# Kernel optimization log

Measured on AMD Instinct MI355X. Metric: run time of the kernel, lower is better.

Reference implementation:

```python
import jax, jax.numpy as jnp
import numpy as np
import math

N, B, D, K = 2000, 2000, 32, 3  # nodes, bills, dim, order+1


def setup_inputs() -> dict:
    key = jax.random.key(0)
    ks = jax.random.split(key, 6)
    return {
        "events": jax.random.randint(ks[0], (N, B), 0, 2) > 0,          # [N,B] bool votes
        "events_time": jax.random.uniform(ks[1], (B,), dtype=jnp.float32),  # [B] bill times
        "beta": jax.random.uniform(ks[2], (B,), dtype=jnp.float32),     # bill bias
        "gamma": jax.random.uniform(ks[3], (N,), dtype=jnp.float32),    # politician bias
        "z_b": jax.random.uniform(ks[4], (B, D), dtype=jnp.float32),    # bill embeddings
        "z_p": jax.random.uniform(ks[5], (K, N, D), dtype=jnp.float32), # stacked order-o politician coeffs
    }


def reference(events, events_time, beta, gamma, z_b, z_p):
    k = z_p.shape[0]
    inv_fact = jnp.asarray([1.0 / math.factorial(o) for o in range(k)], dtype=z_p.dtype)
    # powers[o, b] = t_b**o  (o=0 handled explicitly so grads are safe at t=0)
    powers = jnp.stack(
        [jnp.ones_like(events_time) if o == 0 else events_time ** o for o in range(k)]
    )  # [K,B]
    coeff = powers * inv_fact[:, None]                     # [K,B]  t^o/o!
    pos = jnp.einsum('kb,knd->bnd', coeff, z_p)            # [B,N,D] politician positions at each bill time
    diff = pos - z_b[:, None, :]                           # [B,N,D]
    dist = jnp.sqrt(jnp.sum(diff * diff, axis=-1))         # [B,N] Euclidean distance
    logits = gamma[None, :] + beta[:, None] - dist         # [B,N]
    # log p if voted, log(1-p) otherwise; log(1-sigmoid(x)) == log_sigmoid(-x)
    ll = jnp.where(events.T, jax.nn.log_sigmoid(logits), jax.nn.log_sigmoid(-logits))
    return -jnp.sum(ll)
```

## Files before the change

kernel.cpp:

```cpp
#include <hip/hip_runtime.h>
#include <hip/hip_fp16.h>
#include <math.h>

#define NN    2000
#define NB    2000
#define DD    32
#define NOCT  16
#define TILE  64
#define GDIM  32
#define NPART (GDIM * GDIM)

typedef _Float16 half8   __attribute__((ext_vector_type(8)));
typedef float    float4v __attribute__((ext_vector_type(4)));

__global__ __launch_bounds__(256, 4) void pol2vec_main(
    const int*   __restrict__ events,
    const float* __restrict__ tarr,
    const float* __restrict__ beta,
    const float* __restrict__ gamma,
    const float* __restrict__ zb,
    const float* __restrict__ zp,
    float*       __restrict__ partials)
{
    __shared__ _Float16 sW[NOCT * TILE * 8];
    __shared__ _Float16 sZ[NOCT * TILE * 8];
    __shared__ float    sT[TILE][4][6];
    __shared__ float    sT2[TILE][4];
    __shared__ float    s_red[4];

    const int tid  = threadIdx.x;
    const int lane = tid & 63;
    const int w    = tid >> 6;
    const int b0   = blockIdx.x * TILE;
    const int n0   = blockIdx.y * TILE;
    const int wr   = (w >> 1) * 32;
    const int wc   = (w & 1) * 32;
    const int l15  = lane & 15;
    const int l4   = lane >> 4;

    unsigned evb = 0u, vb = 0u;
#pragma unroll
    for (int nr = 0; nr < 2; ++nr)
#pragma unroll
    for (int bc = 0; bc < 2; ++bc)
#pragma unroll
    for (int r = 0; r < 4; ++r) {
        const int ng = n0 + wr + 16 * nr + l4 * 4 + r;
        const int bg = b0 + wc + 16 * bc + l15;
        const bool v = (ng < NN) && (bg < NB);
        const size_t idx = v ? ((size_t)ng * NB + bg) : 0;
        const unsigned bit = 1u << (nr * 8 + bc * 4 + r);
        if (v) vb |= bit;
        if (v && events[idx]) evb |= bit;
    }

    for (int u = tid; u < NOCT * TILE; u += 256) {
        const int oct = u >> 6, nl = u & 63;
        const int n = n0 + nl;
        half8 hv = {};
        if (oct < 12 && n < NN) {
            const float* src = zp + ((size_t)(oct >> 2) * NN + n) * DD + 8 * (oct & 3);
            const float4 x = ((const float4*)src)[0];
            const float4 y = ((const float4*)src)[1];
            hv[0] = (_Float16)x.x; hv[1] = (_Float16)x.y;
            hv[2] = (_Float16)x.z; hv[3] = (_Float16)x.w;
            hv[4] = (_Float16)y.x; hv[5] = (_Float16)y.y;
            hv[6] = (_Float16)y.z; hv[7] = (_Float16)y.w;
        }
        *(half8*)(sW + (size_t)u * 8) = hv;
    }
    for (int u = tid; u < NOCT * TILE; u += 256) {
        const int oct = u >> 6, bl = u & 63;
        const int b = b0 + bl;
        half8 hv = {};
        if (oct < 12 && b < NB) {
            const float t = tarr[b];
            const float s = (oct < 4) ? 1.f : (oct < 8) ? t : 0.5f * t * t;
            const float* src = zb + (size_t)b * DD + 8 * (oct & 3);
            const float4 x = ((const float4*)src)[0];
            const float4 y = ((const float4*)src)[1];
            hv[0] = (_Float16)(s * x.x); hv[1] = (_Float16)(s * x.y);
            hv[2] = (_Float16)(s * x.z); hv[3] = (_Float16)(s * x.w);
            hv[4] = (_Float16)(s * y.x); hv[5] = (_Float16)(s * y.y);
            hv[6] = (_Float16)(s * y.z); hv[7] = (_Float16)(s * y.w);
        }
        *(half8*)(sZ + (size_t)u * 8) = hv;
    }

    {
        const int nl = tid >> 2, q = tid & 3;
        const int n = n0 + nl;
        float aa = 0.f, ab = 0.f, ac = 0.f, bb = 0.f, bc2 = 0.f, cc6 = 0.f;
        if (n < NN) {
            const float* pA = zp + (size_t)n * DD + 8 * q;
            const float* pB = zp + ((size_t)NN + n) * DD + 8 * q;
            const float* pC = zp + ((size_t)2 * NN + n) * DD + 8 * q;
#pragma unroll
            for (int d = 0; d < 8; ++d) {
                const float a = pA[d], b = pB[d], c = pC[d];
                aa = fmaf(a, a, aa); ab = fmaf(a, b, ab); ac = fmaf(a, c, ac);
                bb = fmaf(b, b, bb); bc2 = fmaf(b, c, bc2); cc6 = fmaf(c, c, cc6);
            }
        }
        sT[nl][q][0] = aa;  sT[nl][q][1] = ab;  sT[nl][q][2] = ac;
        sT[nl][q][3] = bb;  sT[nl][q][4] = bc2; sT[nl][q][5] = cc6;
    }
    {
        const int bl = tid >> 2, q = tid & 3;
        const int b = b0 + bl;
        float z2p = 0.f;
        if (b < NB) {
            const float* zr = zb + (size_t)b * DD + 8 * q;
#pragma unroll
            for (int d = 0; d < 8; ++d) z2p = fmaf(zr[d], zr[d], z2p);
        }
        sT2[bl][q] = z2p;
    }
    __syncthreads();

    if (tid < TILE) {
        const int nl = tid;
        float c6[6];
#pragma unroll
        for (int i = 0; i < 6; ++i)
            c6[i] = (sT[nl][0][i] + sT[nl][1][i]) + (sT[nl][2][i] + sT[nl][3][i]);
        half8 hv = {};
        hv[0] = (_Float16)c6[0];
        hv[1] = (_Float16)(2.f * c6[1]);
        hv[2] = (_Float16)(c6[3] + c6[2]);
        hv[3] = (_Float16)c6[4];
        hv[4] = (_Float16)(0.25f * c6[5]);
        hv[5] = (_Float16)1.f;
        *(half8*)(sW + ((size_t)12 * TILE + nl) * 8) = hv;
    } else if (tid < 2 * TILE) {
        const int bl = tid - TILE;
        const int b = b0 + bl;
        const float z2 = (sT2[bl][0] + sT2[bl][1]) + (sT2[bl][2] + sT2[bl][3]);
        const float t = (b < NB) ? tarr[b] : 0.f;
        const float t2 = t * t;
        half8 hv = {};
        hv[0] = (_Float16)(-0.5f);
        hv[1] = (_Float16)(-0.5f * t);
        hv[2] = (_Float16)(-0.5f * t2);
        hv[3] = (_Float16)(-0.5f * t2 * t);
        hv[4] = (_Float16)(-0.5f * t2 * t2);
        hv[5] = (_Float16)(-0.5f * z2);
        *(half8*)(sZ + ((size_t)12 * TILE + bl) * 8) = hv;
    }
    __syncthreads();

    half8 af[2][4], bf[2][4];
#pragma unroll
    for (int ks = 0; ks < 4; ++ks) {
        const int oct = 4 * ks + l4;
#pragma unroll
        for (int h = 0; h < 2; ++h) {
            af[h][ks] = *(const half8*)(sW + ((size_t)oct * TILE + wr + 16 * h + l15) * 8);
            bf[h][ks] = *(const half8*)(sZ + ((size_t)oct * TILE + wc + 16 * h + l15) * 8);
        }
    }

    float4v acc[2][2] = {};
#pragma unroll
    for (int nr = 0; nr < 2; ++nr)
#pragma unroll
    for (int bc = 0; bc < 2; ++bc)
#pragma unroll
    for (int ks = 0; ks < 4; ++ks)
        acc[nr][bc] = __builtin_amdgcn_mfma_f32_16x16x32_f16(
            af[nr][ks], bf[bc][ks], acc[nr][bc], 0, 0, 0);

    float accs = 0.f;
#pragma unroll
    for (int bc = 0; bc < 2; ++bc) {
        const int bg = b0 + wc + 16 * bc + l15;
        const float be = beta[bg < NB ? bg : 0];
#pragma unroll
        for (int nr = 0; nr < 2; ++nr) {
#pragma unroll
            for (int r = 0; r < 4; ++r) {
                const int ng = n0 + wr + 16 * nr + l4 * 4 + r;
                const float g = gamma[ng < NN ? ng : 0];
                const float d2 = fmaxf(-2.f * acc[nr][bc][r], 0.f);
                const float L  = g + be - sqrtf(d2);
                const unsigned bit = 1u << (nr * 8 + bc * 4 + r);
                const float sgn = (evb & bit) ? 1.f : -1.f;
                const float s   = sgn * L;
                const float term = fmaxf(-s, 0.f) + __logf(1.f + __expf(-fabsf(s)));
                accs += (vb & bit) ? term : 0.f;
            }
        }
    }

#pragma unroll
    for (int o = 32; o > 0; o >>= 1) accs += __shfl_down(accs, o, 64);
    if (lane == 0) s_red[w] = accs;
    __syncthreads();
    if (tid == 0)
        partials[blockIdx.y * GDIM + blockIdx.x] =
            (s_red[0] + s_red[1]) + (s_red[2] + s_red[3]);
}

__global__ __launch_bounds__(256) void pol2vec_reduce(
    const float4* __restrict__ p4, float* __restrict__ out)
{
    __shared__ float s_red[4];
    const int tid = threadIdx.x;
    const float4 v = p4[tid];
    float s = (v.x + v.y) + (v.z + v.w);
#pragma unroll
    for (int o = 32; o > 0; o >>= 1) s += __shfl_down(s, o, 64);
    if ((tid & 63) == 0) s_red[tid >> 6] = s;
    __syncthreads();
    if (tid == 0) out[0] = (s_red[0] + s_red[1]) + (s_red[2] + s_red[3]);
}

extern "C" void kernel_launch(void* const* d_in, const int* in_sizes, int n_in,
                              void* d_out, int out_size, void* d_ws, size_t ws_size,
                              hipStream_t stream) {
    const int*   events = (const int*)d_in[0];
    const float* tarr   = (const float*)d_in[1];
    const float* beta   = (const float*)d_in[2];
    const float* gamma  = (const float*)d_in[3];
    const float* zb     = (const float*)d_in[4];
    const float* zp     = (const float*)d_in[5];
    float* out = (float*)d_out;

    float* parts = (float*)d_ws;

    dim3 grid(GDIM, GDIM);
    pol2vec_main<<<grid, 256, 0, stream>>>(events, tarr, beta, gamma, zb, zp,
                                           parts);
    pol2vec_reduce<<<1, 256, 0, stream>>>((const float4*)parts, out);
}
```

Baseline: 25.19 us.

## Fuse operand staging with norm computation and replace reduce kernel with atomics

Staging of the fp16 politician and bill operands into shared memory now reuses the same float4 global loads to compute the per-row Gram terms and the bill norms. The partial sums are combined with warp shuffles instead of a shared-memory scratch array, which removes one barrier and the redundant re-reads of z_p and z_b. The separate final reduction kernel is replaced by a memset plus one atomicAdd per block into the output. This trades a launch for atomic contention, and the summation order becomes nondeterministic.

```diff
diff --git a/kernel.cpp b/kernel.cpp
--- a/kernel.cpp
+++ b/kernel.cpp
@@ -8,10 +8,19 @@
 #define NOCT  16
 #define TILE  64
 #define GDIM  32
-#define NPART (GDIM * GDIM)
 
 typedef _Float16 half8   __attribute__((ext_vector_type(8)));
+typedef _Float16 half4   __attribute__((ext_vector_type(4)));
 typedef float    float4v __attribute__((ext_vector_type(4)));
+
+__device__ __forceinline__ float dot4(const float4 a, const float4 b) {
+    return fmaf(a.x, b.x, fmaf(a.y, b.y, fmaf(a.z, b.z, a.w * b.w)));
+}
+__device__ __forceinline__ half4 cvt4(const float x, const float y,
+                                      const float z, const float w) {
+    half4 h; h[0] = (_Float16)x; h[1] = (_Float16)y;
+    h[2] = (_Float16)z; h[3] = (_Float16)w; return h;
+}
 
 __global__ __launch_bounds__(256, 4) void pol2vec_main(
     const int*   __restrict__ events,
@@ -20,12 +29,10 @@
     const float* __restrict__ gamma,
     const float* __restrict__ zb,
     const float* __restrict__ zp,
-    float*       __restrict__ partials)
+    float*       __restrict__ out)
 {
     __shared__ _Float16 sW[NOCT * TILE * 8];
     __shared__ _Float16 sZ[NOCT * TILE * 8];
-    __shared__ float    sT[TILE][4][6];
-    __shared__ float    sT2[TILE][4];
     __shared__ float    s_red[4];
 
     const int tid  = threadIdx.x;
@@ -54,98 +61,85 @@
         if (v && events[idx]) evb |= bit;
     }
 
-    for (int u = tid; u < NOCT * TILE; u += 256) {
-        const int oct = u >> 6, nl = u & 63;
-        const int n = n0 + nl;
-        half8 hv = {};
-        if (oct < 12 && n < NN) {
-            const float* src = zp + ((size_t)(oct >> 2) * NN + n) * DD + 8 * (oct & 3);
-            const float4 x = ((const float4*)src)[0];
-            const float4 y = ((const float4*)src)[1];
-            hv[0] = (_Float16)x.x; hv[1] = (_Float16)x.y;
-            hv[2] = (_Float16)x.z; hv[3] = (_Float16)x.w;
-            hv[4] = (_Float16)y.x; hv[5] = (_Float16)y.y;
-            hv[6] = (_Float16)y.z; hv[7] = (_Float16)y.w;
-        }
-        *(half8*)(sW + (size_t)u * 8) = hv;
-    }
-    for (int u = tid; u < NOCT * TILE; u += 256) {
-        const int oct = u >> 6, bl = u & 63;
-        const int b = b0 + bl;
-        half8 hv = {};
-        if (oct < 12 && b < NB) {
-            const float t = tarr[b];
-            const float s = (oct < 4) ? 1.f : (oct < 8) ? t : 0.5f * t * t;
-            const float* src = zb + (size_t)b * DD + 8 * (oct & 3);
-            const float4 x = ((const float4*)src)[0];
-            const float4 y = ((const float4*)src)[1];
-            hv[0] = (_Float16)(s * x.x); hv[1] = (_Float16)(s * x.y);
-            hv[2] = (_Float16)(s * x.z); hv[3] = (_Float16)(s * x.w);
-            hv[4] = (_Float16)(s * y.x); hv[5] = (_Float16)(s * y.y);
-            hv[6] = (_Float16)(s * y.z); hv[7] = (_Float16)(s * y.w);
-        }
-        *(half8*)(sZ + (size_t)u * 8) = hv;
-    }
-
-    {
-        const int nl = tid >> 2, q = tid & 3;
-        const int n = n0 + nl;
-        float aa = 0.f, ab = 0.f, ac = 0.f, bb = 0.f, bc2 = 0.f, cc6 = 0.f;
+    if (tid < 3 * TILE) {
+        const half8 zz = {};
+        *(half8*)(sW + ((size_t)(13 * TILE + tid)) * 8) = zz;
+        *(half8*)(sZ + ((size_t)(13 * TILE + tid)) * 8) = zz;
+    }
+
+    const int row = tid >> 3;
+    const int q   = tid & 7;
+    const int hs  = (q & 1) * 4;
+
+#pragma unroll
+    for (int p = 0; p < 2; ++p) {
+        const int nl = 32 * p + row;
+        const int n  = n0 + nl;
+        float4 a4 = {0.f,0.f,0.f,0.f}, b4 = {0.f,0.f,0.f,0.f}, c4 = {0.f,0.f,0.f,0.f};
         if (n < NN) {
-            const float* pA = zp + (size_t)n * DD + 8 * q;
-            const float* pB = zp + ((size_t)NN + n) * DD + 8 * q;
-            const float* pC = zp + ((size_t)2 * NN + n) * DD + 8 * q;
-#pragma unroll
-            for (int d = 0; d < 8; ++d) {
-                const float a = pA[d], b = pB[d], c = pC[d];
-                aa = fmaf(a, a, aa); ab = fmaf(a, b, ab); ac = fmaf(a, c, ac);
-                bb = fmaf(b, b, bb); bc2 = fmaf(b, c, bc2); cc6 = fmaf(c, c, cc6);
-            }
-        }
-        sT[nl][q][0] = aa;  sT[nl][q][1] = ab;  sT[nl][q][2] = ac;
-        sT[nl][q][3] = bb;  sT[nl][q][4] = bc2; sT[nl][q][5] = cc6;
-    }
-    {
-        const int bl = tid >> 2, q = tid & 3;
-        const int b = b0 + bl;
-        float z2p = 0.f;
+            a4 = ((const float4*)(zp + (size_t)n * DD))[q];
+            b4 = ((const float4*)(zp + ((size_t)NN + n) * DD))[q];
+            c4 = ((const float4*)(zp + ((size_t)2 * NN + n) * DD))[q];
+        }
+        *(half4*)(sW + ((size_t)((0 + (q >> 1)) * TILE + nl)) * 8 + hs) =
+            cvt4(a4.x, a4.y, a4.z, a4.w);
+        *(half4*)(sW + ((size_t)((4 + (q >> 1)) * TILE + nl)) * 8 + hs) =
+            cvt4(b4.x, b4.y, b4.z, b4.w);
+        *(half4*)(sW + ((size_t)((8 + (q >> 1)) * TILE + nl)) * 8 + hs) =
+            cvt4(c4.x, c4.y, c4.z, c4.w);
+
+        float paa = dot4(a4, a4), pab = dot4(a4, b4), pac = dot4(a4, c4);
+        float pbb = dot4(b4, b4), pbc = dot4(b4, c4), pcc = dot4(c4, c4);
+#pragma unroll
+        for (int off = 1; off < 8; off <<= 1) {
+            paa += __shfl_xor(paa, off); pab += __shfl_xor(pab, off);
+            pac += __shfl_xor(pac, off); pbb += __shfl_xor(pbb, off);
+            pbc += __shfl_xor(pbc, off); pcc += __shfl_xor(pcc, off);
+        }
+        if (q == 0) {
+            half8 hv = {};
+            hv[0] = (_Float16)paa;
+            hv[1] = (_Float16)(2.f * pab);
+            hv[2] = (_Float16)(pbb + pac);
+            hv[3] = (_Float16)pbc;
+            hv[4] = (_Float16)(0.25f * pcc);
+            hv[5] = (_Float16)1.f;
+            *(half8*)(sW + ((size_t)(12 * TILE + nl)) * 8) = hv;
+        }
+    }
+
+#pragma unroll
+    for (int p = 0; p < 2; ++p) {
+        const int bl = 32 * p + row;
+        const int b  = b0 + bl;
+        float4 z4 = {0.f,0.f,0.f,0.f};
+        float t = 0.f;
         if (b < NB) {
-            const float* zr = zb + (size_t)b * DD + 8 * q;
-#pragma unroll
-            for (int d = 0; d < 8; ++d) z2p = fmaf(zr[d], zr[d], z2p);
-        }
-        sT2[bl][q] = z2p;
-    }
-    __syncthreads();
-
-    if (tid < TILE) {
-        const int nl = tid;
-        float c6[6];
-#pragma unroll
-        for (int i = 0; i < 6; ++i)
-            c6[i] = (sT[nl][0][i] + sT[nl][1][i]) + (sT[nl][2][i] + sT[nl][3][i]);
-        half8 hv = {};
-        hv[0] = (_Float16)c6[0];
-        hv[1] = (_Float16)(2.f * c6[1]);
-        hv[2] = (_Float16)(c6[3] + c6[2]);
-        hv[3] = (_Float16)c6[4];
-        hv[4] = (_Float16)(0.25f * c6[5]);
-        hv[5] = (_Float16)1.f;
-        *(half8*)(sW + ((size_t)12 * TILE + nl) * 8) = hv;
-    } else if (tid < 2 * TILE) {
-        const int bl = tid - TILE;
-        const int b = b0 + bl;
-        const float z2 = (sT2[bl][0] + sT2[bl][1]) + (sT2[bl][2] + sT2[bl][3]);
-        const float t = (b < NB) ? tarr[b] : 0.f;
-        const float t2 = t * t;
-        half8 hv = {};
-        hv[0] = (_Float16)(-0.5f);
-        hv[1] = (_Float16)(-0.5f * t);
-        hv[2] = (_Float16)(-0.5f * t2);
-        hv[3] = (_Float16)(-0.5f * t2 * t);
-        hv[4] = (_Float16)(-0.5f * t2 * t2);
-        hv[5] = (_Float16)(-0.5f * z2);
-        *(half8*)(sZ + ((size_t)12 * TILE + bl) * 8) = hv;
+            z4 = ((const float4*)(zb + (size_t)b * DD))[q];
+            t  = tarr[b];
+        }
+        const float th = 0.5f * t * t;
+        *(half4*)(sZ + ((size_t)((0 + (q >> 1)) * TILE + bl)) * 8 + hs) =
+            cvt4(z4.x, z4.y, z4.z, z4.w);
+        *(half4*)(sZ + ((size_t)((4 + (q >> 1)) * TILE + bl)) * 8 + hs) =
+            cvt4(t * z4.x, t * z4.y, t * z4.z, t * z4.w);
+        *(half4*)(sZ + ((size_t)((8 + (q >> 1)) * TILE + bl)) * 8 + hs) =
+            cvt4(th * z4.x, th * z4.y, th * z4.z, th * z4.w);
+
+        float pz2 = dot4(z4, z4);
+#pragma unroll
+        for (int off = 1; off < 8; off <<= 1) pz2 += __shfl_xor(pz2, off);
+        if (q == 0) {
+            const float t2 = t * t;
+            half8 hv = {};
+            hv[0] = (_Float16)(-0.5f);
+            hv[1] = (_Float16)(-0.5f * t);
+            hv[2] = (_Float16)(-0.5f * t2);
+            hv[3] = (_Float16)(-0.5f * t2 * t);
+            hv[4] = (_Float16)(-0.5f * t2 * t2);
+            hv[5] = (_Float16)(-0.5f * pz2);
+            *(half8*)(sZ + ((size_t)(12 * TILE + bl)) * 8) = hv;
+        }
     }
     __syncthreads();
 
@@ -197,22 +191,7 @@
     if (lane == 0) s_red[w] = accs;
     __syncthreads();
     if (tid == 0)
-        partials[blockIdx.y * GDIM + blockIdx.x] =
-            (s_red[0] + s_red[1]) + (s_red[2] + s_red[3]);
-}
-
-__global__ __launch_bounds__(256) void pol2vec_reduce(
-    const float4* __restrict__ p4, float* __restrict__ out)
-{
-    __shared__ float s_red[4];
-    const int tid = threadIdx.x;
-    const float4 v = p4[tid];
-    float s = (v.x + v.y) + (v.z + v.w);
-#pragma unroll
-    for (int o = 32; o > 0; o >>= 1) s += __shfl_down(s, o, 64);
-    if ((tid & 63) == 0) s_red[tid >> 6] = s;
-    __syncthreads();
-    if (tid == 0) out[0] = (s_red[0] + s_red[1]) + (s_red[2] + s_red[3]);
+        atomicAdd(out, (s_red[0] + s_red[1]) + (s_red[2] + s_red[3]));
 }
 
 extern "C" void kernel_launch(void* const* d_in, const int* in_sizes, int n_in,
@@ -226,10 +205,9 @@
     const float* zp     = (const float*)d_in[5];
     float* out = (float*)d_out;
 
-    float* parts = (float*)d_ws;
+    hipMemsetAsync(out, 0, (size_t)out_size * sizeof(float), stream);
 
     dim3 grid(GDIM, GDIM);
     pol2vec_main<<<grid, 256, 0, stream>>>(events, tarr, beta, gamma, zb, zp,
-                                           parts);
-    pol2vec_reduce<<<1, 256, 0, stream>>>((const float4*)parts, out);
-}
+                                           out);
+}
```

Result: slower. 31.42 us (+24.7%).
